# Kernel tuning notes

Hardware: AMD Instinct MI355X
Metric: run time of the kernel (lower is better)

The kernel has to match this reference:

```python
import jax, jax.numpy as jnp
import numpy as np

POS_IOU_THR = 0.7
NEG_IOU_THR = 0.3
MIN_POS_IOU = 0.3
MATCH_LOW_QUALITY = True

N_BOXES = 500000
N_GTS = 128
DIM = 3  # 3D boxes -> 6 coords


def _make_boxes(key, n, max_size):
    k1, k2 = jax.random.split(key)
    lt = jax.random.uniform(k1, (n, DIM)) * (1.0 - max_size)
    sz = jax.random.uniform(k2, (n, DIM)) * max_size + 1e-3
    return jnp.concatenate([lt, lt + sz], axis=-1)  # [n, 2*DIM], valid lt < rb


def setup_inputs() -> dict:
    key = jax.random.key(0)
    kb, kg, kl = jax.random.split(key, 3)
    bboxes = _make_boxes(kb, N_BOXES, 0.15)
    gt_bboxes = _make_boxes(kg, N_GTS, 0.15)
    gt_labels = jax.random.randint(kl, (N_GTS,), 1, 21, dtype=jnp.int32)
    return {"bboxes": bboxes, "gt_bboxes": gt_bboxes, "gt_labels": gt_labels}


def _iou_nd(b1, b2):
    # b1: [N, 2d], b2: [M, 2d] -> [N, M] axis-aligned IoU in d dims
    d = b1.shape[-1] // 2
    lt = jnp.maximum(b1[:, None, :d], b2[None, :, :d])   # [N, M, d]
    rb = jnp.minimum(b1[:, None, d:], b2[None, :, d:])
    inter = jnp.prod(jnp.clip(rb - lt, 0.0), axis=-1)    # [N, M]
    a1 = jnp.prod(b1[:, d:] - b1[:, :d], axis=-1)        # [N]
    a2 = jnp.prod(b2[:, d:] - b2[:, :d], axis=-1)        # [M]
    return inter / (a1[:, None] + a2[None, :] - inter + 1e-7)


def reference(bboxes, gt_bboxes, gt_labels):
    num_bboxes, num_gts = bboxes.shape[0], gt_bboxes.shape[0]
    iou = _iou_nd(bboxes, gt_bboxes)                      # [N, M]

    anchors_iou_max = jnp.max(iou, axis=1)                # [N]
    anchors_iou_argmax = jnp.argmax(iou, axis=1)          # [N]
    gt_iou_max = jnp.max(iou, axis=0)                     # [M]
    gt_iou_argmax = jnp.argmax(iou, axis=0)               # [M]

    # -1 ignore, 0 negative, n>0 matched gt (1-based)
    assigned = jnp.full((num_bboxes,), -1, dtype=jnp.int32)
    assigned = jnp.where(anchors_iou_max < NEG_IOU_THR, 0, assigned)
    assigned = jnp.where(anchors_iou_max >= POS_IOU_THR,
                         anchors_iou_argmax.astype(jnp.int32) + 1, assigned)

    if MATCH_LOW_QUALITY:
        # torch loop: for i in range(M): if gt_iou_max[i] >= min_pos_iou:
        cand = jnp.where(gt_iou_max >= MIN_POS_IOU,
                         jnp.arange(1, num_gts + 1, dtype=jnp.int32), 0)
        override = jnp.zeros((num_bboxes,), dtype=jnp.int32).at[gt_iou_argmax].max(cand)
        assigned = jnp.where(override > 0, override, assigned)

    pos_mask = assigned > 0
    gi = jnp.clip(assigned - 1, 0)                        # safe gather index
    assigned_labels = jnp.where(pos_mask, gt_labels[gi],
                                jnp.where(assigned == 0, 0, -1)).astype(jnp.int32)
    assigned_bboxes = jnp.where(pos_mask[:, None], gt_bboxes[gi],
                                jnp.full_like(bboxes, -1.0))
    return assigned_labels, assigned_bboxes
```

## Files before the change

### kernel.cpp

```cpp
#include <hip/hip_runtime.h>


#define MMAX 128

#define IOU_CHAIN(X0, Y0, Z0, X1, Y1, Z1, AR, BEST, ARG, ENC)                  \
    {                                                                          \
        float cx = fmaxf(__fsub_rn(fminf(X1, glo.w), fmaxf(X0, glo.x)), 0.f);  \
        float cy = fmaxf(__fsub_rn(fminf(Y1, ghi.x), fmaxf(Y0, glo.y)), 0.f);  \
        float cz = fmaxf(__fsub_rn(fminf(Z1, ghi.y), fmaxf(Z0, glo.z)), 0.f);  \
        float inter = __fmul_rn(__fmul_rn(cx, cy), cz);                        \
        if (inter > 0.f) {                                 \
            float den = __fadd_rn(__fsub_rn(__fadd_rn(AR, ghi.z), inter), 1e-7f);\
            float iou = __fdiv_rn(inter, den);                                 \
            if (iou > BEST) { BEST = iou; ARG = g; }                           \
            if (iou >= 0.3f) {                                                 \
                unsigned long long enc =                                       \
                    ((unsigned long long)__float_as_uint(iou) << 32) |         \
                    (unsigned long long)(ENC);                                 \
                atomicMax(&lsl[g], enc);                                       \
            }                                                                  \
        }                                                                      \
    }

template <int MC>
__global__ __launch_bounds__(256) void iou_main(
    const float* __restrict__ bx, const float* __restrict__ gt,
    const int* __restrict__ gl,
    float* __restrict__ out_lab, float* __restrict__ out_bb,
    unsigned long long* __restrict__ slots,
    int N, int Mrt)
{
    const int M = MC ? MC : Mrt;
    const int tid = threadIdx.x;

    __shared__ float4 gb4[MMAX * 2];
    __shared__ unsigned long long lsl[MMAX];
    if (tid < M) {
        const float* gp = gt + (size_t)tid * 6;
        float x0 = gp[0], y0 = gp[1], z0 = gp[2];
        float x1 = gp[3], y1 = gp[4], z1 = gp[5];
        float area = __fmul_rn(__fmul_rn(__fsub_rn(x1, x0), __fsub_rn(y1, y0)),
                               __fsub_rn(z1, z0));
        gb4[2 * tid]     = make_float4(x0, y0, z0, x1);
        gb4[2 * tid + 1] = make_float4(y1, z1, area, (float)gl[tid]);
    }
    if (tid < MMAX) lsl[tid] = 0ULL;
    __syncthreads();

    const int H = (N + 1) >> 1;
    const int a = blockIdx.x * 256 + tid;
    const int b = a + H;
    const bool va = (a < H);
    const bool vb = va && (b < N);

    float ax0 = 0.f, ay0 = 0.f, az0 = 0.f, ax1 = 0.f, ay1 = 0.f, az1 = 0.f;
    if (va) { const float* p = bx + (size_t)a * 6;
        ax0 = p[0]; ay0 = p[1]; az0 = p[2]; ax1 = p[3]; ay1 = p[4]; az1 = p[5]; }
    float bx0 = 0.f, by0 = 0.f, bz0 = 0.f, bx1 = 0.f, by1 = 0.f, bz1 = 0.f;
    if (vb) { const float* p = bx + (size_t)b * 6;
        bx0 = p[0]; by0 = p[1]; bz0 = p[2]; bx1 = p[3]; by1 = p[4]; bz1 = p[5]; }

    const float a1a = __fmul_rn(__fmul_rn(__fsub_rn(ax1, ax0),
                       __fsub_rn(ay1, ay0)), __fsub_rn(az1, az0));
    const float a1b = __fmul_rn(__fmul_rn(__fsub_rn(bx1, bx0),
                       __fsub_rn(by1, by0)), __fsub_rn(bz1, bz0));

    const unsigned encA = 0xFFFFFFFFu - (unsigned)a;
    const unsigned encB = 0xFFFFFFFFu - (unsigned)b;

    float bestA = 0.f, bestB = 0.f;
    int   argA = 0,    argB = 0;

    for (int g = 0; g < M; ++g) {
        const float4 glo = gb4[2 * g];
        const float4 ghi = gb4[2 * g + 1];
        IOU_CHAIN(ax0, ay0, az0, ax1, ay1, az1, a1a, bestA, argA, encA)
        IOU_CHAIN(bx0, by0, bz0, bx1, by1, bz1, a1b, bestB, argB, encB)
    }

    const float* gbf = (const float*)gb4;
    if (va) {
        float lab;
        if (bestA >= 0.7f) lab = gbf[8 * argA + 7];
        else               lab = (bestA < 0.3f) ? 0.f : -1.f;
        out_lab[a] = lab;
        float* ob = out_bb + (size_t)a * 6;
        if (bestA >= 0.7f) {
            ob[0] = gbf[8*argA+0]; ob[1] = gbf[8*argA+1]; ob[2] = gbf[8*argA+2];
            ob[3] = gbf[8*argA+3]; ob[4] = gbf[8*argA+4]; ob[5] = gbf[8*argA+5];
        } else {
            ob[0] = -1.f; ob[1] = -1.f; ob[2] = -1.f;
            ob[3] = -1.f; ob[4] = -1.f; ob[5] = -1.f;
        }
    }
    if (vb) {
        float lab;
        if (bestB >= 0.7f) lab = gbf[8 * argB + 7];
        else               lab = (bestB < 0.3f) ? 0.f : -1.f;
        out_lab[b] = lab;
        float* ob = out_bb + (size_t)b * 6;
        if (bestB >= 0.7f) {
            ob[0] = gbf[8*argB+0]; ob[1] = gbf[8*argB+1]; ob[2] = gbf[8*argB+2];
            ob[3] = gbf[8*argB+3]; ob[4] = gbf[8*argB+4]; ob[5] = gbf[8*argB+5];
        } else {
            ob[0] = -1.f; ob[1] = -1.f; ob[2] = -1.f;
            ob[3] = -1.f; ob[4] = -1.f; ob[5] = -1.f;
        }
    }

    __syncthreads();
    for (int g = tid; g < M; g += 256) {
        unsigned long long v = lsl[g];
        if (v) atomicMax(&slots[g], v);
    }
}

__global__ __launch_bounds__(MMAX) void iou_override(
    const float* __restrict__ gt, const int* __restrict__ gl,
    const unsigned long long* __restrict__ slots,
    float* __restrict__ out_lab, float* __restrict__ out_bb, int M)
{
    __shared__ int s_anchor[MMAX];
    __shared__ int s_cand[MMAX];
    const int i = threadIdx.x;

    int anchor = -1, cand = 0;
    if (i < M) {
        unsigned long long v = slots[i];
        if (v != 0ULL) {
            anchor = (int)(0xFFFFFFFFu - (unsigned)(v & 0xFFFFFFFFu));
            cand   = i + 1;
        }
    }
    s_anchor[i] = anchor;
    s_cand[i]   = cand;
    __syncthreads();

    if (cand > 0) {
        bool win = true;
        for (int j = 0; j < M; ++j)
            if (s_cand[j] > cand && s_anchor[j] == anchor) { win = false; break; }
        if (win) {
            out_lab[anchor] = (float)gl[i];
            float* ob = out_bb + (size_t)anchor * 6;
            const float* gp = gt + (size_t)i * 6;
            ob[0] = gp[0]; ob[1] = gp[1]; ob[2] = gp[2];
            ob[3] = gp[3]; ob[4] = gp[4]; ob[5] = gp[5];
        }
    }
}

extern "C" void kernel_launch(void* const* d_in, const int* in_sizes, int n_in,
                              void* d_out, int out_size, void* d_ws, size_t ws_size,
                              hipStream_t stream)
{
    const float* bx = (const float*)d_in[0];
    const float* gt = (const float*)d_in[1];
    const int*   gl = (const int*)d_in[2];
    const int N = in_sizes[0] / 6;
    int M = in_sizes[1] / 6;
    if (M > MMAX) M = MMAX;

    float* out_lab = (float*)d_out;
    float* out_bb  = (float*)d_out + N;

    unsigned long long* slots = (unsigned long long*)d_ws;

    hipMemsetAsync(d_ws, 0, MMAX * 8, stream);

    const int H = (N + 1) / 2;
    const int nblocks = (H + 255) / 256;

    if (M == MMAX) {
        hipLaunchKernelGGL(iou_main<MMAX>, dim3(nblocks), dim3(256), 0, stream,
                           bx, gt, gl, out_lab, out_bb, slots, N, M);
    } else {
        hipLaunchKernelGGL(iou_main<0>, dim3(nblocks), dim3(256), 0, stream,
                           bx, gt, gl, out_lab, out_bb, slots, N, M);
    }
    hipLaunchKernelGGL(iou_override, dim3(1), dim3(MMAX), 0, stream,
                       gt, gl, slots, out_lab, out_bb, M);
}
```

Before: 70.98 us.

## Split GT loop across wavefronts with four anchors per lane and shared-memory argmax reduction

Each block now covers 64 anchor positions, each taken at four strided offsets, and its four wavefronts each scan a quarter of the ground-truth boxes. Per-anchor best IoU and argmax are merged through 64-bit atomicMax in shared memory, with the argmax encoded inverted so the lowest index wins ties, and one thread per anchor then writes the outputs. The goal is more independent work per lane to expose ILP and a shorter serial GT loop per thread. The cost is extra LDS atomics, a second barrier, and higher register pressure from four anchor states.

```diff
diff --git a/kernel.cpp b/kernel.cpp
--- a/kernel.cpp
+++ b/kernel.cpp
@@ -31,10 +31,13 @@
     int N, int Mrt)
 {
     const int M = MC ? MC : Mrt;
-    const int tid = threadIdx.x;
+    const int tid  = threadIdx.x;
+    const int lane = tid & 63;
+    const int wv   = tid >> 6;
 
     __shared__ float4 gb4[MMAX * 2];
     __shared__ unsigned long long lsl[MMAX];
+    __shared__ unsigned long long asl[256];
     if (tid < M) {
         const float* gp = gt + (size_t)tid * 6;
         float x0 = gp[0], y0 = gp[1], z0 = gp[2];
@@ -45,13 +48,16 @@
         gb4[2 * tid + 1] = make_float4(y1, z1, area, (float)gl[tid]);
     }
     if (tid < MMAX) lsl[tid] = 0ULL;
+    asl[tid] = 0ULL;
     __syncthreads();
 
-    const int H = (N + 1) >> 1;
-    const int a = blockIdx.x * 256 + tid;
-    const int b = a + H;
-    const bool va = (a < H);
+    const int H = (N + 3) >> 2;
+    const int base = blockIdx.x * 64 + lane;
+    const int a = base, b = base + H, c = base + 2 * H, d = base + 3 * H;
+    const bool va = (base < H);
     const bool vb = va && (b < N);
+    const bool vc = va && (c < N);
+    const bool vd = va && (d < N);
 
     float ax0 = 0.f, ay0 = 0.f, az0 = 0.f, ax1 = 0.f, ay1 = 0.f, az1 = 0.f;
     if (va) { const float* p = bx + (size_t)a * 6;
@@ -59,59 +65,84 @@
     float bx0 = 0.f, by0 = 0.f, bz0 = 0.f, bx1 = 0.f, by1 = 0.f, bz1 = 0.f;
     if (vb) { const float* p = bx + (size_t)b * 6;
         bx0 = p[0]; by0 = p[1]; bz0 = p[2]; bx1 = p[3]; by1 = p[4]; bz1 = p[5]; }
+    float cx0 = 0.f, cy0 = 0.f, cz0 = 0.f, cx1 = 0.f, cy1 = 0.f, cz1 = 0.f;
+    if (vc) { const float* p = bx + (size_t)c * 6;
+        cx0 = p[0]; cy0 = p[1]; cz0 = p[2]; cx1 = p[3]; cy1 = p[4]; cz1 = p[5]; }
+    float dx0 = 0.f, dy0 = 0.f, dz0 = 0.f, dx1 = 0.f, dy1 = 0.f, dz1 = 0.f;
+    if (vd) { const float* p = bx + (size_t)d * 6;
+        dx0 = p[0]; dy0 = p[1]; dz0 = p[2]; dx1 = p[3]; dy1 = p[4]; dz1 = p[5]; }
 
     const float a1a = __fmul_rn(__fmul_rn(__fsub_rn(ax1, ax0),
                        __fsub_rn(ay1, ay0)), __fsub_rn(az1, az0));
     const float a1b = __fmul_rn(__fmul_rn(__fsub_rn(bx1, bx0),
                        __fsub_rn(by1, by0)), __fsub_rn(bz1, bz0));
+    const float a1c = __fmul_rn(__fmul_rn(__fsub_rn(cx1, cx0),
+                       __fsub_rn(cy1, cy0)), __fsub_rn(cz1, cz0));
+    const float a1d = __fmul_rn(__fmul_rn(__fsub_rn(dx1, dx0),
+                       __fsub_rn(dy1, dy0)), __fsub_rn(dz1, dz0));
 
     const unsigned encA = 0xFFFFFFFFu - (unsigned)a;
     const unsigned encB = 0xFFFFFFFFu - (unsigned)b;
-
-    float bestA = 0.f, bestB = 0.f;
-    int   argA = 0,    argB = 0;
-
-    for (int g = 0; g < M; ++g) {
+    const unsigned encC = 0xFFFFFFFFu - (unsigned)c;
+    const unsigned encD = 0xFFFFFFFFu - (unsigned)d;
+
+    const int chunk = (M + 3) >> 2;
+    const int g0 = wv * chunk;
+    const int g1 = (g0 + chunk < M) ? (g0 + chunk) : M;
+
+    float bestA = 0.f, bestB = 0.f, bestC = 0.f, bestD = 0.f;
+    int   argA = g0,   argB = g0,   argC = g0,   argD = g0;
+
+    for (int g = g0; g < g1; ++g) {
         const float4 glo = gb4[2 * g];
         const float4 ghi = gb4[2 * g + 1];
         IOU_CHAIN(ax0, ay0, az0, ax1, ay1, az1, a1a, bestA, argA, encA)
         IOU_CHAIN(bx0, by0, bz0, bx1, by1, bz1, a1b, bestB, argB, encB)
-    }
-
-    const float* gbf = (const float*)gb4;
-    if (va) {
-        float lab;
-        if (bestA >= 0.7f) lab = gbf[8 * argA + 7];
-        else               lab = (bestA < 0.3f) ? 0.f : -1.f;
-        out_lab[a] = lab;
-        float* ob = out_bb + (size_t)a * 6;
-        if (bestA >= 0.7f) {
-            ob[0] = gbf[8*argA+0]; ob[1] = gbf[8*argA+1]; ob[2] = gbf[8*argA+2];
-            ob[3] = gbf[8*argA+3]; ob[4] = gbf[8*argA+4]; ob[5] = gbf[8*argA+5];
-        } else {
-            ob[0] = -1.f; ob[1] = -1.f; ob[2] = -1.f;
-            ob[3] = -1.f; ob[4] = -1.f; ob[5] = -1.f;
+        IOU_CHAIN(cx0, cy0, cz0, cx1, cy1, cz1, a1c, bestC, argC, encC)
+        IOU_CHAIN(dx0, dy0, dz0, dx1, dy1, dz1, a1d, bestD, argD, encD)
+    }
+
+    if (va) atomicMax(&asl[0 * 64 + lane],
+        ((unsigned long long)__float_as_uint(bestA) << 32) |
+        (unsigned long long)(0xFFFFFFFFu - (unsigned)argA));
+    if (vb) atomicMax(&asl[1 * 64 + lane],
+        ((unsigned long long)__float_as_uint(bestB) << 32) |
+        (unsigned long long)(0xFFFFFFFFu - (unsigned)argB));
+    if (vc) atomicMax(&asl[2 * 64 + lane],
+        ((unsigned long long)__float_as_uint(bestC) << 32) |
+        (unsigned long long)(0xFFFFFFFFu - (unsigned)argC));
+    if (vd) atomicMax(&asl[3 * 64 + lane],
+        ((unsigned long long)__float_as_uint(bestD) << 32) |
+        (unsigned long long)(0xFFFFFFFFu - (unsigned)argD));
+    __syncthreads();
+
+    if (tid < M) {
+        unsigned long long v = lsl[tid];
+        if (v) atomicMax(&slots[tid], v);
+    }
+
+    {
+        const int k = tid >> 6, l = tid & 63;
+        const int sb = blockIdx.x * 64 + l;
+        const int anchor = sb + k * H;
+        if (sb < H && anchor < N) {
+            const unsigned long long v = asl[tid];
+            const float best = __uint_as_float((unsigned)(v >> 32));
+            const int garg = (int)(0xFFFFFFFFu - (unsigned)(v & 0xFFFFFFFFu));
+            const float* gbf = (const float*)gb4;
+            float lab;
+            if (best >= 0.7f) lab = gbf[8 * garg + 7];
+            else              lab = (best < 0.3f) ? 0.f : -1.f;
+            out_lab[anchor] = lab;
+            float* ob = out_bb + (size_t)anchor * 6;
+            if (best >= 0.7f) {
+                ob[0] = gbf[8*garg+0]; ob[1] = gbf[8*garg+1]; ob[2] = gbf[8*garg+2];
+                ob[3] = gbf[8*garg+3]; ob[4] = gbf[8*garg+4]; ob[5] = gbf[8*garg+5];
+            } else {
+                ob[0] = -1.f; ob[1] = -1.f; ob[2] = -1.f;
+                ob[3] = -1.f; ob[4] = -1.f; ob[5] = -1.f;
+            }
         }
-    }
-    if (vb) {
-        float lab;
-        if (bestB >= 0.7f) lab = gbf[8 * argB + 7];
-        else               lab = (bestB < 0.3f) ? 0.f : -1.f;
-        out_lab[b] = lab;
-        float* ob = out_bb + (size_t)b * 6;
-        if (bestB >= 0.7f) {
-            ob[0] = gbf[8*argB+0]; ob[1] = gbf[8*argB+1]; ob[2] = gbf[8*argB+2];
-            ob[3] = gbf[8*argB+3]; ob[4] = gbf[8*argB+4]; ob[5] = gbf[8*argB+5];
-        } else {
-            ob[0] = -1.f; ob[1] = -1.f; ob[2] = -1.f;
-            ob[3] = -1.f; ob[4] = -1.f; ob[5] = -1.f;
-        }
-    }
-
-    __syncthreads();
-    for (int g = tid; g < M; g += 256) {
-        unsigned long long v = lsl[g];
-        if (v) atomicMax(&slots[g], v);
     }
 }
 
@@ -168,8 +199,8 @@
 
     hipMemsetAsync(d_ws, 0, MMAX * 8, stream);
 
-    const int H = (N + 1) / 2;
-    const int nblocks = (H + 255) / 256;
+    const int H = (N + 3) / 4;
+    const int nblocks = (H + 63) / 64;
 
     if (M == MMAX) {
         hipLaunchKernelGGL(iou_main<MMAX>, dim3(nblocks), dim3(256), 0, stream,
```

New measurement: 67.38 us. 5.1% less time.
